# Kernel optimization log

Measured on AMD Instinct MI355X. Metric: run time of the kernel, lower is better.

The kernel has to match this reference:

```python
import jax, jax.numpy as jnp
import numpy as np

B, N, C, NH = 8, 16384, 256, 8
CH = C // NH          # head dim = 32
SCALE = CH ** -0.5
HH = WW = 128         # N = HH*WW
# CoaT crpe window dict {3:2, 5:3, 7:3}: 2 heads->3x3, 3 heads->5x5, 3 heads->7x7


def setup_inputs() -> dict:
    key = jax.random.key(0)
    ks = jax.random.split(key, 9)
    w = lambda k, shp: (jax.random.normal(k, shp, jnp.float32) * 0.02)
    return {
        "x": jax.random.normal(ks[0], (B, N, C), jnp.float32),
        "w_qkv": w(ks[1], (C, 3 * C)),              # qkv_bias=False
        "w_proj": w(ks[2], (C, C)),
        "b_proj": jnp.zeros((C,), jnp.float32),
        "w3": w(ks[3], (3, 3, 1, 2 * CH)),          # HWIO depthwise, 2 heads
        "b3": jnp.zeros((2 * CH,), jnp.float32),
        "w5": w(ks[4], (5, 5, 1, 3 * CH)),          # 3 heads
        "b5": jnp.zeros((3 * CH,), jnp.float32),
        "w7": w(ks[5], (7, 7, 1, 3 * CH)),          # 3 heads
        "b7": jnp.zeros((3 * CH,), jnp.float32),
        "H": HH,
        "W": WW,
    }


def _hydra(q, k, v):
    # q,k,v: [B, h, N, Ch]; normalize over feature dim, O(N) token reduction
    qn = q * jax.lax.rsqrt(jnp.sum(q * q, axis=-1, keepdims=True))
    kn = k * jax.lax.rsqrt(jnp.sum(k * k, axis=-1, keepdims=True))
    kv = jnp.sum(kn * v, axis=-2, keepdims=True)   # [B, h, 1, Ch]
    return qn * kv                                  # broadcast over tokens


def _dwconv(img, kern, bias):
    # img: [B, c, H, W]; kern: [kh, kw, 1, c] (HWIO depthwise)
    c = img.shape[1]
    out = jax.lax.conv_general_dilated(
        img, kern, window_strides=(1, 1), padding="SAME",
        feature_group_count=c,
        dimension_numbers=("NCHW", "HWIO", "NCHW"))
    return out + bias[None, :, None, None]


def _crpe(q, v, Hs, Ws, convs):
    # CoaT ConvRelPosEnc: depthwise conv on v per head group, gated by q
    b, h, n, ch = v.shape
    outs, idx = [], 0
    for heads, kern, bias in convs:
        vs = v[:, idx:idx + heads]                          # [B, hs, N, Ch]
        v_img = vs.transpose(0, 1, 3, 2).reshape(b, heads * ch, Hs, Ws)
        cv = _dwconv(v_img, kern, bias)
        cv = cv.reshape(b, heads, ch, n).transpose(0, 1, 3, 2)
        outs.append(q[:, idx:idx + heads] * cv)
        idx += heads
    return jnp.concatenate(outs, axis=1)                    # [B, h, N, Ch]


def reference(x, w_qkv, w_proj, b_proj, w3, b3, w5, b5, w7, b7, H, W):
    b, n, c = x.shape
    qkv = (x @ w_qkv).reshape(b, n, 3, NH, CH).transpose(2, 0, 3, 1, 4)
    q, k, v = qkv[0], qkv[1], qkv[2]                        # [B, h, N, Ch]
    factor_att = _hydra(q, k, v)
    crpe = _crpe(q, v, H, W, [(2, w3, b3), (3, w5, b5), (3, w7, b7)])
    out = SCALE * factor_att + crpe
    out = out.transpose(0, 2, 1, 3).reshape(b, n, c)        # [B, N, C]
    return out @ w_proj + b_proj
```

## Files before the change

kernel.cpp:

```cpp
#include <hip/hip_runtime.h>
#include <hip/hip_bf16.h>


typedef __hip_bfloat16 bf16;
typedef __bf16 bf16x8 __attribute__((ext_vector_type(8)));
typedef unsigned short u16x8 __attribute__((ext_vector_type(8)));
typedef float f32x4 __attribute__((ext_vector_type(4)));
typedef float f32x8 __attribute__((ext_vector_type(8)));

#define SCALE_ 0.17677669529663687f

__device__ __forceinline__ unsigned short f2b(float f) {
  __hip_bfloat16 h = __float2bfloat16(f);
  return __builtin_bit_cast(unsigned short, h);
}
__device__ __forceinline__ float blo(unsigned u) {
  return __builtin_bit_cast(float, u << 16);
}
__device__ __forceinline__ float bhi(unsigned u) {
  return __builtin_bit_cast(float, u & 0xffff0000u);
}
__device__ __forceinline__ f32x8 unpack8(uint4 u) {
  f32x8 r;
  r[0] = blo(u.x); r[1] = bhi(u.x); r[2] = blo(u.y); r[3] = bhi(u.y);
  r[4] = blo(u.z); r[5] = bhi(u.z); r[6] = blo(u.w); r[7] = bhi(u.w);
  return r;
}
__device__ __forceinline__ uint4 pack8(float a0, float a1, float a2, float a3,
                                       float a4, float a5, float a6, float a7) {
  uint4 s;
  s.x = (unsigned)f2b(a0) | ((unsigned)f2b(a1) << 16);
  s.y = (unsigned)f2b(a2) | ((unsigned)f2b(a3) << 16);
  s.z = (unsigned)f2b(a4) | ((unsigned)f2b(a5) << 16);
  s.w = (unsigned)f2b(a6) | ((unsigned)f2b(a7) << 16);
  return s;
}
__device__ __forceinline__ void gload16(const void* g, void* l) {
  __builtin_amdgcn_global_load_lds(
      (const __attribute__((address_space(1))) unsigned int*)g,
      (__attribute__((address_space(3))) unsigned int*)l, 16, 0, 0);
}
__device__ __forceinline__ f32x4 mfma16(u16x8 a, u16x8 b, f32x4 c) {
  return __builtin_amdgcn_mfma_f32_16x16x32_bf16(
      __builtin_bit_cast(bf16x8, a), __builtin_bit_cast(bf16x8, b), c, 0, 0, 0);
}

__global__ __launch_bounds__(256) void prep_weights(
    const float* __restrict__ wqkv, const float* __restrict__ wproj,
    bf16* __restrict__ wqkvT, bf16* __restrict__ wprojT) {
  const int idx = blockIdx.x * 256 + threadIdx.x;
  if (idx < 768 * 256) {
    const int j = idx >> 8, k = idx & 255;
    wqkvT[idx] = __float2bfloat16(wqkv[k * 768 + j]);
  }
  if (idx < 256 * 256) {
    const int j = idx >> 8, k = idx & 255;
    wprojT[idx] = __float2bfloat16(wproj[k * 256 + j]);
  }
}

__global__ __launch_bounds__(256) void qkv_mfma(
    const float* __restrict__ x, const bf16* __restrict__ wT,
    bf16* __restrict__ qO, bf16* __restrict__ kO, bf16* __restrict__ vO) {
  __shared__ __align__(16) char As[16384];
  __shared__ __align__(16) char Bs[16384];
  const int tid = threadIdx.x;
  const int l = tid & 63, w = tid >> 6;
  const int wr = w >> 1, wc = w & 1;

  const int lin = blockIdx.y * 6 + blockIdx.x;
  const int xcd = lin & 7, qq = lin >> 3;
  const int jt = qq % 6;
  const int ttile = xcd * 128 + qq / 6;
  const int j0 = jt << 7;
  const int t0 = ttile << 7;

  f32x4 acc[4][4];
#pragma unroll
  for (int m = 0; m < 4; ++m)
#pragma unroll
    for (int t = 0; t < 4; ++t) acc[m][t] = (f32x4){0.f, 0.f, 0.f, 0.f};

  const int arow0 = w * 16 + (l >> 2), arow1 = arow0 + 64;
  const int asl = l & 3;
  const bf16* asrc0 = wT + (size_t)(j0 + arow0) * 256 + ((asl ^ (arow0 & 3)) << 3);
  const bf16* asrc1 = wT + (size_t)(j0 + arow1) * 256 + ((asl ^ (arow1 & 3)) << 3);
  const int ad0 = w * 1024;
  const int ad1 = 4096 + w * 1024;

  const int brow = tid >> 1, bkh = tid & 1;
  const float* xp = x + (size_t)(t0 + brow) * 256 + bkh * 16;
  const int bw0 = brow * 64 + (((bkh << 1) ^ (brow & 3)) << 4);
  const int bw1 = brow * 64 + ((((bkh << 1) | 1) ^ (brow & 3)) << 4);

  const int fr = l & 15;
  const int fs = ((l >> 4) ^ (l & 3)) << 4;

  {
    const float4 xa0 = *(const float4*)(xp);
    const float4 xa1 = *(const float4*)(xp + 4);
    const float4 xa2 = *(const float4*)(xp + 8);
    const float4 xa3 = *(const float4*)(xp + 12);
    gload16(asrc0, As + ad0);
    gload16(asrc1, As + ad1);
    u16x8 p0, p1;
    p0[0] = f2b(xa0.x); p0[1] = f2b(xa0.y); p0[2] = f2b(xa0.z); p0[3] = f2b(xa0.w);
    p0[4] = f2b(xa1.x); p0[5] = f2b(xa1.y); p0[6] = f2b(xa1.z); p0[7] = f2b(xa1.w);
    p1[0] = f2b(xa2.x); p1[1] = f2b(xa2.y); p1[2] = f2b(xa2.z); p1[3] = f2b(xa2.w);
    p1[4] = f2b(xa3.x); p1[5] = f2b(xa3.y); p1[6] = f2b(xa3.z); p1[7] = f2b(xa3.w);
    *(u16x8*)(Bs + bw0) = p0;
    *(u16x8*)(Bs + bw1) = p1;
  }
  __syncthreads();

  int cur = 0;
  for (int t = 0; t < 8; ++t) {
    const int kn = (t + 1) << 5;
    const int nxt = (cur ^ 1) << 13;
    float4 xa0, xa1, xa2, xa3;
    if (t < 7) {
      xa0 = *(const float4*)(xp + kn);
      xa1 = *(const float4*)(xp + kn + 4);
      xa2 = *(const float4*)(xp + kn + 8);
      xa3 = *(const float4*)(xp + kn + 12);
      gload16(asrc0 + kn, As + nxt + ad0);
      gload16(asrc1 + kn, As + nxt + ad1);
    }
    const char* Ac = As + (cur << 13);
    const char* Bc = Bs + (cur << 13);
    u16x8 af[4], bfv[4];
#pragma unroll
    for (int m = 0; m < 4; ++m)
      af[m] = *(const u16x8*)(Ac + (wr * 64 + m * 16 + fr) * 64 + fs);
#pragma unroll
    for (int tt = 0; tt < 4; ++tt)
      bfv[tt] = *(const u16x8*)(Bc + (wc * 64 + tt * 16 + fr) * 64 + fs);
#pragma unroll
    for (int m = 0; m < 4; ++m)
#pragma unroll
      for (int tt = 0; tt < 4; ++tt)
        acc[m][tt] = mfma16(af[m], bfv[tt], acc[m][tt]);
    if (t < 7) {
      u16x8 p0, p1;
      p0[0] = f2b(xa0.x); p0[1] = f2b(xa0.y); p0[2] = f2b(xa0.z); p0[3] = f2b(xa0.w);
      p0[4] = f2b(xa1.x); p0[5] = f2b(xa1.y); p0[6] = f2b(xa1.z); p0[7] = f2b(xa1.w);
      p1[0] = f2b(xa2.x); p1[1] = f2b(xa2.y); p1[2] = f2b(xa2.z); p1[3] = f2b(xa2.w);
      p1[4] = f2b(xa3.x); p1[5] = f2b(xa3.y); p1[6] = f2b(xa3.z); p1[7] = f2b(xa3.w);
      *(u16x8*)(Bs + nxt + bw0) = p0;
      *(u16x8*)(Bs + nxt + bw1) = p1;
    }
    __syncthreads();
    cur ^= 1;
  }

  const int region = j0 >> 8;
  bf16* outp = (region == 0) ? qO : ((region == 1) ? kO : vO);
  const int b = t0 >> 14;
  const int n0 = (t0 & 16383) + wc * 64;
  const int fq = l >> 4;
  const int jl = (j0 & 255) + wr * 64;
#pragma unroll
  for (int m = 0; m < 4; ++m) {
    const int j = jl + m * 16 + fq * 4;
#pragma unroll
    for (int t = 0; t < 4; ++t) {
      const int n = n0 + t * 16 + fr;
      uint2 pk;
      pk.x = (unsigned)f2b(acc[m][t][0]) | ((unsigned)f2b(acc[m][t][1]) << 16);
      pk.y = (unsigned)f2b(acc[m][t][2]) | ((unsigned)f2b(acc[m][t][3]) << 16);
      *(uint2*)&outp[((size_t)b * 16384 + n) * 256 + j] = pk;
    }
  }
}

__global__ __launch_bounds__(256) void kv_reduce(
    const bf16* __restrict__ kT, const bf16* __restrict__ vT,
    float* __restrict__ kv) {
  const int tid = threadIdx.x;
  const int bh = blockIdx.y;
  const int b = bh >> 3, h = bh & 7;
  f32x8 part[4];
#pragma unroll
  for (int cc = 0; cc < 4; ++cc) part[cc] = (f32x8)0.f;

  for (int it = 0; it < 4; ++it) {
    const int n = blockIdx.x * 1024 + it * 256 + tid;
    const size_t off = ((size_t)b * 16384 + n) * 256 + h * 32;
    const uint4* kp = (const uint4*)(kT + off);
    const uint4* vp = (const uint4*)(vT + off);
    f32x8 kf[4];
    float ss = 0.f;
#pragma unroll
    for (int cc = 0; cc < 4; ++cc) {
      kf[cc] = unpack8(kp[cc]);
#pragma unroll
      for (int i = 0; i < 8; ++i) ss += kf[cc][i] * kf[cc][i];
    }
    const float inv = rsqrtf(ss);
#pragma unroll
    for (int cc = 0; cc < 4; ++cc) {
      f32x8 vf = unpack8(vp[cc]);
#pragma unroll
      for (int i = 0; i < 8; ++i) part[cc][i] += kf[cc][i] * inv * vf[i];
    }
  }
#pragma unroll
  for (int cc = 0; cc < 4; ++cc)
#pragma unroll
    for (int i = 0; i < 8; ++i) {
      float p = part[cc][i];
#pragma unroll
      for (int off = 32; off >= 1; off >>= 1) p += __shfl_xor(p, off);
      part[cc][i] = p;
    }
  if ((tid & 63) == 0) {
#pragma unroll
    for (int cc = 0; cc < 4; ++cc)
#pragma unroll
      for (int i = 0; i < 8; ++i)
        atomicAdd(&kv[bh * 32 + cc * 8 + i], part[cc][i]);
  }
}

template <int K>
__global__ __launch_bounds__(256) void crpe_conv(
    const bf16* __restrict__ qT, const bf16* __restrict__ vT,
    const float* __restrict__ kvbuf, const float* __restrict__ wp,
    const float* __restrict__ bp, int OC, int hbase,
    bf16* __restrict__ mid) {
  constexpr int R = K / 2;
  constexpr int S = 16 + 2 * R;
  constexpr int NSLOT = 4 * ((S - 1) * 23 + 1);
  __shared__ __align__(16) char vs[NSLOT * 16];
  __shared__ float wlds[K * K * 32];
  __shared__ float blds[32];

  const int tid = threadIdx.x;
  const int hg = blockIdx.x;
  const int h = hbase + hg;
  const int tile = blockIdx.y;
  const int b = blockIdx.z;
  const int tx0 = (tile & 7) * 16, ty0 = (tile >> 3) * 16;
  const int px = tid & 15, py = tid >> 4;
  const int ocbase = hg * 32;

  for (int e = tid; e < S * S; e += 256) {
    const int ly = e / S, lx = e - ly * S;
    const int gy = ty0 - R + ly, gx = tx0 - R + lx;
    uint4 d0 = {0, 0, 0, 0}, d1 = {0, 0, 0, 0}, d2 = {0, 0, 0, 0},
          d3 = {0, 0, 0, 0};
    if (gy >= 0 && gy < 128 && gx >= 0 && gx < 128) {
      const uint4* src = (const uint4*)(vT +
          ((size_t)b * 16384 + gy * 128 + gx) * 256 + h * 32);
      d0 = src[0]; d1 = src[1]; d2 = src[2]; d3 = src[3];
    }
    const int p = ly * 22 + lx;
    const int sw = (p >> 1) & 3;
    char* base = vs + ((p << 2) << 4);
    *(uint4*)(base + ((0 ^ sw) << 4)) = d0;
    *(uint4*)(base + ((1 ^ sw) << 4)) = d1;
    *(uint4*)(base + ((2 ^ sw) << 4)) = d2;
    *(uint4*)(base + ((3 ^ sw) << 4)) = d3;
  }
  for (int e = tid; e < K * K * 32; e += 256)
    wlds[e] = wp[(e >> 5) * OC + ocbase + (e & 31)];
  if (tid < 32) blds[tid] = bp[ocbase + tid];
  __syncthreads();

  const float4* bl4 = (const float4*)blds;
  f32x8 acc[4];
#pragma unroll
  for (int cc = 0; cc < 4; ++cc) {
    const float4 b0 = bl4[cc * 2], b1 = bl4[cc * 2 + 1];
    acc[cc][0] = b0.x; acc[cc][1] = b0.y; acc[cc][2] = b0.z; acc[cc][3] = b0.w;
    acc[cc][4] = b1.x; acc[cc][5] = b1.y; acc[cc][6] = b1.z; acc[cc][7] = b1.w;
  }
  const float4* wlds4 = (const float4*)wlds;
#pragma unroll 1
  for (int ky = 0; ky < K; ++ky) {
#pragma unroll
    for (int kx = 0; kx < K; ++kx) {
      const int p = (py + ky) * 22 + (px + kx);
      const int tap = ky * K + kx;
      const int sw = (p >> 1) & 3;
      const char* base = vs + ((p << 2) << 4);
#pragma unroll
      for (int cc = 0; cc < 4; ++cc) {
        const uint4 vv = *(const uint4*)(base + ((cc ^ sw) << 4));
        const f32x8 vf = unpack8(vv);
        const float4 w0 = wlds4[tap * 8 + cc * 2];
        const float4 w1 = wlds4[tap * 8 + cc * 2 + 1];
        acc[cc][0] += vf[0] * w0.x; acc[cc][1] += vf[1] * w0.y;
        acc[cc][2] += vf[2] * w0.z; acc[cc][3] += vf[3] * w0.w;
        acc[cc][4] += vf[4] * w1.x; acc[cc][5] += vf[5] * w1.y;
        acc[cc][6] += vf[6] * w1.z; acc[cc][7] += vf[7] * w1.w;
      }
    }
  }

  const int n = (ty0 + py) * 128 + (tx0 + px);
  const size_t off = ((size_t)b * 16384 + n) * 256 + h * 32;
  const uint4* qsrc = (const uint4*)(qT + off);
  f32x8 qv[4];
  float ss = 0.f;
#pragma unroll
  for (int cc = 0; cc < 4; ++cc) {
    qv[cc] = unpack8(qsrc[cc]);
#pragma unroll
    for (int i = 0; i < 8; ++i) ss += qv[cc][i] * qv[cc][i];
  }
  const float qinv = rsqrtf(ss);
  const float4* kvp = (const float4*)(kvbuf + ((size_t)b * 8 + h) * 32);
  uint4* mdst = (uint4*)(mid + off);
#pragma unroll
  for (int cc = 0; cc < 4; ++cc) {
    const float4 ka = kvp[cc * 2], kb = kvp[cc * 2 + 1];
    float o[8];
    o[0] = SCALE_ * qv[cc][0] * qinv * ka.x + qv[cc][0] * acc[cc][0];
    o[1] = SCALE_ * qv[cc][1] * qinv * ka.y + qv[cc][1] * acc[cc][1];
    o[2] = SCALE_ * qv[cc][2] * qinv * ka.z + qv[cc][2] * acc[cc][2];
    o[3] = SCALE_ * qv[cc][3] * qinv * ka.w + qv[cc][3] * acc[cc][3];
    o[4] = SCALE_ * qv[cc][4] * qinv * kb.x + qv[cc][4] * acc[cc][4];
    o[5] = SCALE_ * qv[cc][5] * qinv * kb.y + qv[cc][5] * acc[cc][5];
    o[6] = SCALE_ * qv[cc][6] * qinv * kb.z + qv[cc][6] * acc[cc][6];
    o[7] = SCALE_ * qv[cc][7] * qinv * kb.w + qv[cc][7] * acc[cc][7];
    mdst[cc] = pack8(o[0], o[1], o[2], o[3], o[4], o[5], o[6], o[7]);
  }
}

__global__ __launch_bounds__(256) void proj_mfma(
    const bf16* __restrict__ mid, const bf16* __restrict__ wpT,
    const float* __restrict__ bproj, float* __restrict__ out) {
  __shared__ __align__(16) char As[16384];
  __shared__ __align__(16) char Bs[16384];
  const int tid = threadIdx.x;
  const int l = tid & 63, w = tid >> 6;
  const int wr = w >> 1, wc = w & 1;

  const int lin = blockIdx.y * 2 + blockIdx.x;
  const int xcd = lin & 7, qq = lin >> 3;
  const int jt = qq & 1;
  const int ttile = xcd * 128 + (qq >> 1);
  const int j0 = jt << 7;
  const int tk0 = ttile << 7;

  f32x4 acc[4][4];
#pragma unroll
  for (int m = 0; m < 4; ++m)
#pragma unroll
    for (int t = 0; t < 4; ++t) acc[m][t] = (f32x4){0.f, 0.f, 0.f, 0.f};

  const int row0 = w * 16 + (l >> 2), row1 = row0 + 64;
  const int sl = l & 3;
  const bf16* asrc0 = wpT + (size_t)(j0 + row0) * 256 + ((sl ^ (row0 & 3)) << 3);
  const bf16* asrc1 = wpT + (size_t)(j0 + row1) * 256 + ((sl ^ (row1 & 3)) << 3);
  const bf16* bsrc0 = mid + (size_t)(tk0 + row0) * 256 + ((sl ^ (row0 & 3)) << 3);
  const bf16* bsrc1 = mid + (size_t)(tk0 + row1) * 256 + ((sl ^ (row1 & 3)) << 3);
  const int d0 = w * 1024;
  const int d1 = 4096 + w * 1024;

  const int fr = l & 15;
  const int fs = ((l >> 4) ^ (l & 3)) << 4;

  gload16(asrc0, As + d0);
  gload16(asrc1, As + d1);
  gload16(bsrc0, Bs + d0);
  gload16(bsrc1, Bs + d1);
  __syncthreads();

  int cur = 0;
  for (int t = 0; t < 8; ++t) {
    const int kn = (t + 1) << 5;
    const int nxt = (cur ^ 1) << 13;
    if (t < 7) {
      gload16(asrc0 + kn, As + nxt + d0);
      gload16(asrc1 + kn, As + nxt + d1);
      gload16(bsrc0 + kn, Bs + nxt + d0);
      gload16(bsrc1 + kn, Bs + nxt + d1);
    }
    const char* Ac = As + (cur << 13);
    const char* Bc = Bs + (cur << 13);
    u16x8 af[4], bfv[4];
#pragma unroll
    for (int m = 0; m < 4; ++m)
      af[m] = *(const u16x8*)(Ac + (wr * 64 + m * 16 + fr) * 64 + fs);
#pragma unroll
    for (int tt = 0; tt < 4; ++tt)
      bfv[tt] = *(const u16x8*)(Bc + (wc * 64 + tt * 16 + fr) * 64 + fs);
#pragma unroll
    for (int m = 0; m < 4; ++m)
#pragma unroll
      for (int tt = 0; tt < 4; ++tt)
        acc[m][tt] = mfma16(af[m], bfv[tt], acc[m][tt]);
    __syncthreads();
    cur ^= 1;
  }

  const int fq = l >> 4;
#pragma unroll
  for (int m = 0; m < 4; ++m) {
    const int j = j0 + wr * 64 + m * 16 + fq * 4;
    const float4 bias = *(const float4*)&bproj[j];
#pragma unroll
    for (int t = 0; t < 4; ++t) {
      const int token = tk0 + wc * 64 + t * 16 + fr;
      float4 r;
      r.x = acc[m][t][0] + bias.x;
      r.y = acc[m][t][1] + bias.y;
      r.z = acc[m][t][2] + bias.z;
      r.w = acc[m][t][3] + bias.w;
      *(float4*)&out[(size_t)token * 256 + j] = r;
    }
  }
}

extern "C" void kernel_launch(void* const* d_in, const int* in_sizes, int n_in,
                              void* d_out, int out_size, void* d_ws,
                              size_t ws_size, hipStream_t stream) {
  const float* x     = (const float*)d_in[0];
  const float* wqkv  = (const float*)d_in[1];
  const float* wproj = (const float*)d_in[2];
  const float* bproj = (const float*)d_in[3];
  const float* w3 = (const float*)d_in[4];
  const float* b3 = (const float*)d_in[5];
  const float* w5 = (const float*)d_in[6];
  const float* b5 = (const float*)d_in[7];
  const float* w7 = (const float*)d_in[8];
  const float* b7 = (const float*)d_in[9];
  float* out = (float*)d_out;

  const size_t PLANE = (size_t)8 * 16384 * 256;
  bf16* qT  = (bf16*)d_ws;
  bf16* vT  = qT + PLANE;
  bf16* kT  = vT + PLANE;
  bf16* mid = kT;
  float* kv = (float*)(kT + PLANE);
  bf16* wqkvT  = (bf16*)(kv + 2048);
  bf16* wprojT = wqkvT + 768 * 256;

  hipMemsetAsync(kv, 0, 2048 * sizeof(float), stream);
  prep_weights<<<dim3(768), 256, 0, stream>>>(wqkv, wproj, wqkvT, wprojT);
  qkv_mfma<<<dim3(6, 1024), 256, 0, stream>>>(x, wqkvT, qT, kT, vT);
  kv_reduce<<<dim3(16, 64), 256, 0, stream>>>(kT, vT, kv);
  crpe_conv<3><<<dim3(2, 64, 8), 256, 0, stream>>>(qT, vT, kv, w3, b3, 64, 0, mid);
  crpe_conv<5><<<dim3(3, 64, 8), 256, 0, stream>>>(qT, vT, kv, w5, b5, 96, 2, mid);
  crpe_conv<7><<<dim3(3, 64, 8), 256, 0, stream>>>(qT, vT, kv, w7, b7, 96, 5, mid);
  proj_mfma<<<dim3(2, 1024), 256, 0, stream>>>(mid, wprojT, bproj, out);
}
```

Baseline: 420.6 us.

## Stage GEMM epilogues through LDS for coalesced stores; coalesce kv_reduce loads

The QKV and projection GEMM epilogues now write accumulators into a swizzled LDS tile and read them back so each thread emits full 16-byte contiguous row stores, replacing scattered 8/16-byte column fragments. The LDS swizzle for operand tiles is changed to use (row>>1)&3 to reduce bank conflicts. kv_reduce is restructured so each warp reads whole 512-byte token rows across all heads, with per-head norms via shuffles and an LDS tree reduction before the atomics. This adds an extra LDS round trip and barriers in the epilogues.

```diff
diff --git a/kernel.cpp b/kernel.cpp
--- a/kernel.cpp
+++ b/kernel.cpp
@@ -62,8 +62,9 @@
 __global__ __launch_bounds__(256) void qkv_mfma(
     const float* __restrict__ x, const bf16* __restrict__ wT,
     bf16* __restrict__ qO, bf16* __restrict__ kO, bf16* __restrict__ vO) {
-  __shared__ __align__(16) char As[16384];
-  __shared__ __align__(16) char Bs[16384];
+  __shared__ __align__(16) char LDSU[32768];
+  char* As = LDSU;
+  char* Bs = LDSU + 16384;
   const int tid = threadIdx.x;
   const int l = tid & 63, w = tid >> 6;
   const int wr = w >> 1, wc = w & 1;
@@ -83,18 +84,22 @@
 
   const int arow0 = w * 16 + (l >> 2), arow1 = arow0 + 64;
   const int asl = l & 3;
-  const bf16* asrc0 = wT + (size_t)(j0 + arow0) * 256 + ((asl ^ (arow0 & 3)) << 3);
-  const bf16* asrc1 = wT + (size_t)(j0 + arow1) * 256 + ((asl ^ (arow1 & 3)) << 3);
+  const bf16* asrc0 =
+      wT + (size_t)(j0 + arow0) * 256 + ((asl ^ ((arow0 >> 1) & 3)) << 3);
+  const bf16* asrc1 =
+      wT + (size_t)(j0 + arow1) * 256 + ((asl ^ ((arow1 >> 1) & 3)) << 3);
   const int ad0 = w * 1024;
   const int ad1 = 4096 + w * 1024;
 
   const int brow = tid >> 1, bkh = tid & 1;
   const float* xp = x + (size_t)(t0 + brow) * 256 + bkh * 16;
-  const int bw0 = brow * 64 + (((bkh << 1) ^ (brow & 3)) << 4);
-  const int bw1 = brow * 64 + ((((bkh << 1) | 1) ^ (brow & 3)) << 4);
+  const int bsw = (brow >> 1) & 3;
+  const int bw0 = brow * 64 + (((bkh << 1) ^ bsw) << 4);
+  const int bw1 = brow * 64 + ((((bkh << 1) | 1) ^ bsw) << 4);
 
   const int fr = l & 15;
-  const int fs = ((l >> 4) ^ (l & 3)) << 4;
+  const int fq = l >> 4;
+  const int fs = (fq ^ ((l >> 1) & 3)) << 4;
 
   {
     const float4 xa0 = *(const float4*)(xp);
@@ -153,72 +158,78 @@
     cur ^= 1;
   }
 
+#pragma unroll
+  for (int m = 0; m < 4; ++m) {
+    const int jq = wr * 16 + m * 4 + fq;
+#pragma unroll
+    for (int t = 0; t < 4; ++t) {
+      const int token = wc * 64 + t * 16 + fr;
+      const int p = jq ^ (token & 15);
+      uint2 pk;
+      pk.x = (unsigned)f2b(acc[m][t][0]) | ((unsigned)f2b(acc[m][t][1]) << 16);
+      pk.y = (unsigned)f2b(acc[m][t][2]) | ((unsigned)f2b(acc[m][t][3]) << 16);
+      *(uint2*)(LDSU + token * 256 + (p << 3)) = pk;
+    }
+  }
+  __syncthreads();
+
   const int region = j0 >> 8;
   bf16* outp = (region == 0) ? qO : ((region == 1) ? kO : vO);
   const int b = t0 >> 14;
-  const int n0 = (t0 & 16383) + wc * 64;
-  const int fq = l >> 4;
-  const int jl = (j0 & 255) + wr * 64;
-#pragma unroll
-  for (int m = 0; m < 4; ++m) {
-    const int j = jl + m * 16 + fq * 4;
-#pragma unroll
-    for (int t = 0; t < 4; ++t) {
-      const int n = n0 + t * 16 + fr;
-      uint2 pk;
-      pk.x = (unsigned)f2b(acc[m][t][0]) | ((unsigned)f2b(acc[m][t][1]) << 16);
-      pk.y = (unsigned)f2b(acc[m][t][2]) | ((unsigned)f2b(acc[m][t][3]) << 16);
-      *(uint2*)&outp[((size_t)b * 16384 + n) * 256 + j] = pk;
-    }
+  const int n0 = t0 & 16383;
+  const int jl = j0 & 255;
+  const int seg = tid & 15;
+#pragma unroll
+  for (int r = 0; r < 8; ++r) {
+    const int token = r * 16 + (tid >> 4);
+    const int tsw = token & 15;
+    const int q0 = (2 * seg) ^ tsw;
+    const int q1 = (2 * seg + 1) ^ tsw;
+    const uint2 lo = *(const uint2*)(LDSU + token * 256 + (q0 << 3));
+    const uint2 hi = *(const uint2*)(LDSU + token * 256 + (q1 << 3));
+    uint4 d;
+    d.x = lo.x; d.y = lo.y; d.z = hi.x; d.w = hi.y;
+    *(uint4*)&outp[((size_t)b * 16384 + n0 + token) * 256 + jl + seg * 8] = d;
   }
 }
 
 __global__ __launch_bounds__(256) void kv_reduce(
     const bf16* __restrict__ kT, const bf16* __restrict__ vT,
     float* __restrict__ kv) {
+  __shared__ float red[256 * 8];
   const int tid = threadIdx.x;
-  const int bh = blockIdx.y;
-  const int b = bh >> 3, h = bh & 7;
-  f32x8 part[4];
-#pragma unroll
-  for (int cc = 0; cc < 4; ++cc) part[cc] = (f32x8)0.f;
-
-  for (int it = 0; it < 4; ++it) {
-    const int n = blockIdx.x * 1024 + it * 256 + tid;
-    const size_t off = ((size_t)b * 16384 + n) * 256 + h * 32;
-    const uint4* kp = (const uint4*)(kT + off);
-    const uint4* vp = (const uint4*)(vT + off);
-    f32x8 kf[4];
+  const int b = blockIdx.y;
+  const int seg = tid & 31;
+  f32x8 part = (f32x8)0.f;
+
+  for (int r = 0; r < 32; ++r) {
+    const int token = blockIdx.x * 256 + r * 8 + (tid >> 5);
+    const size_t roff = ((size_t)b * 16384 + token) * 256;
+    const uint4 kd = *(const uint4*)(kT + roff + seg * 8);
+    const f32x8 kf = unpack8(kd);
     float ss = 0.f;
 #pragma unroll
-    for (int cc = 0; cc < 4; ++cc) {
-      kf[cc] = unpack8(kp[cc]);
-#pragma unroll
-      for (int i = 0; i < 8; ++i) ss += kf[cc][i] * kf[cc][i];
-    }
+    for (int i = 0; i < 8; ++i) ss += kf[i] * kf[i];
+    ss += __shfl_xor(ss, 1);
+    ss += __shfl_xor(ss, 2);
     const float inv = rsqrtf(ss);
-#pragma unroll
-    for (int cc = 0; cc < 4; ++cc) {
-      f32x8 vf = unpack8(vp[cc]);
-#pragma unroll
-      for (int i = 0; i < 8; ++i) part[cc][i] += kf[cc][i] * inv * vf[i];
-    }
-  }
-#pragma unroll
-  for (int cc = 0; cc < 4; ++cc)
-#pragma unroll
-    for (int i = 0; i < 8; ++i) {
-      float p = part[cc][i];
-#pragma unroll
-      for (int off = 32; off >= 1; off >>= 1) p += __shfl_xor(p, off);
-      part[cc][i] = p;
-    }
-  if ((tid & 63) == 0) {
-#pragma unroll
-    for (int cc = 0; cc < 4; ++cc)
-#pragma unroll
-      for (int i = 0; i < 8; ++i)
-        atomicAdd(&kv[bh * 32 + cc * 8 + i], part[cc][i]);
+    const uint4 vd = *(const uint4*)(vT + roff + seg * 8);
+    const f32x8 vf = unpack8(vd);
+#pragma unroll
+    for (int i = 0; i < 8; ++i) part[i] += kf[i] * inv * vf[i];
+  }
+#pragma unroll
+  for (int i = 0; i < 8; ++i) red[tid * 8 + i] = part[i];
+  __syncthreads();
+  if (tid < 32) {
+    f32x8 s = (f32x8)0.f;
+#pragma unroll
+    for (int k = 0; k < 8; ++k)
+#pragma unroll
+      for (int i = 0; i < 8; ++i) s[i] += red[(tid + 32 * k) * 8 + i];
+#pragma unroll
+    for (int i = 0; i < 8; ++i)
+      atomicAdd(&kv[b * 256 + seg * 8 + i], s[i]);
   }
 }
 
@@ -331,8 +342,9 @@
 __global__ __launch_bounds__(256) void proj_mfma(
     const bf16* __restrict__ mid, const bf16* __restrict__ wpT,
     const float* __restrict__ bproj, float* __restrict__ out) {
-  __shared__ __align__(16) char As[16384];
-  __shared__ __align__(16) char Bs[16384];
+  __shared__ __align__(16) char LDSU[32768];
+  char* As = LDSU;
+  char* Bs = LDSU + 16384;
   const int tid = threadIdx.x;
   const int l = tid & 63, w = tid >> 6;
   const int wr = w >> 1, wc = w & 1;
@@ -352,15 +364,17 @@
 
   const int row0 = w * 16 + (l >> 2), row1 = row0 + 64;
   const int sl = l & 3;
-  const bf16* asrc0 = wpT + (size_t)(j0 + row0) * 256 + ((sl ^ (row0 & 3)) << 3);
-  const bf16* asrc1 = wpT + (size_t)(j0 + row1) * 256 + ((sl ^ (row1 & 3)) << 3);
-  const bf16* bsrc0 = mid + (size_t)(tk0 + row0) * 256 + ((sl ^ (row0 & 3)) << 3);
-  const bf16* bsrc1 = mid + (size_t)(tk0 + row1) * 256 + ((sl ^ (row1 & 3)) << 3);
+  const int sw0 = (row0 >> 1) & 3, sw1 = (row1 >> 1) & 3;
+  const bf16* asrc0 = wpT + (size_t)(j0 + row0) * 256 + ((sl ^ sw0) << 3);
+  const bf16* asrc1 = wpT + (size_t)(j0 + row1) * 256 + ((sl ^ sw1) << 3);
+  const bf16* bsrc0 = mid + (size_t)(tk0 + row0) * 256 + ((sl ^ sw0) << 3);
+  const bf16* bsrc1 = mid + (size_t)(tk0 + row1) * 256 + ((sl ^ sw1) << 3);
   const int d0 = w * 1024;
   const int d1 = 4096 + w * 1024;
 
   const int fr = l & 15;
-  const int fs = ((l >> 4) ^ (l & 3)) << 4;
+  const int fq = l >> 4;
+  const int fs = (fq ^ ((l >> 1) & 3)) << 4;
 
   gload16(asrc0, As + d0);
   gload16(asrc1, As + d1);
@@ -396,21 +410,44 @@
     cur ^= 1;
   }
 
-  const int fq = l >> 4;
 #pragma unroll
   for (int m = 0; m < 4; ++m) {
-    const int j = j0 + wr * 64 + m * 16 + fq * 4;
-    const float4 bias = *(const float4*)&bproj[j];
+    const float4 bias = *(const float4*)&bproj[j0 + wr * 64 + m * 16 + fq * 4];
 #pragma unroll
     for (int t = 0; t < 4; ++t) {
-      const int token = tk0 + wc * 64 + t * 16 + fr;
-      float4 r;
-      r.x = acc[m][t][0] + bias.x;
-      r.y = acc[m][t][1] + bias.y;
-      r.z = acc[m][t][2] + bias.z;
-      r.w = acc[m][t][3] + bias.w;
-      *(float4*)&out[(size_t)token * 256 + j] = r;
-    }
+      acc[m][t][0] += bias.x;
+      acc[m][t][1] += bias.y;
+      acc[m][t][2] += bias.z;
+      acc[m][t][3] += bias.w;
+    }
+  }
+
+  for (int chunk = 0; chunk < 2; ++chunk) {
+    if (wc == chunk) {
+#pragma unroll
+      for (int m = 0; m < 4; ++m) {
+        const int jq = wr * 16 + m * 4 + fq;
+#pragma unroll
+        for (int t = 0; t < 4; ++t) {
+          const int ltok = t * 16 + fr;
+          const int p = jq ^ (ltok & 15);
+          float4 r;
+          r.x = acc[m][t][0]; r.y = acc[m][t][1];
+          r.z = acc[m][t][2]; r.w = acc[m][t][3];
+          *(float4*)(LDSU + ltok * 512 + (p << 4)) = r;
+        }
+      }
+    }
+    __syncthreads();
+    const int seg = tid & 31;
+#pragma unroll
+    for (int r = 0; r < 8; ++r) {
+      const int ltok = r * 8 + (tid >> 5);
+      const int p = seg ^ (ltok & 15);
+      const float4 dv = *(const float4*)(LDSU + ltok * 512 + (p << 4));
+      *(float4*)&out[(size_t)(tk0 + chunk * 64 + ltok) * 256 + j0 + seg * 4] = dv;
+    }
+    __syncthreads();
   }
 }
 
@@ -441,7 +478,7 @@
   hipMemsetAsync(kv, 0, 2048 * sizeof(float), stream);
   prep_weights<<<dim3(768), 256, 0, stream>>>(wqkv, wproj, wqkvT, wprojT);
   qkv_mfma<<<dim3(6, 1024), 256, 0, stream>>>(x, wqkvT, qT, kT, vT);
-  kv_reduce<<<dim3(16, 64), 256, 0, stream>>>(kT, vT, kv);
+  kv_reduce<<<dim3(64, 8), 256, 0, stream>>>(kT, vT, kv);
   crpe_conv<3><<<dim3(2, 64, 8), 256, 0, stream>>>(qT, vT, kv, w3, b3, 64, 0, mid);
   crpe_conv<5><<<dim3(3, 64, 8), 256, 0, stream>>>(qT, vT, kv, w5, b5, 96, 2, mid);
   crpe_conv<7><<<dim3(3, 64, 8), 256, 0, stream>>>(qT, vT, kv, w7, b7, 96, 5, mid);
```

Result: faster. 344.8 us (-18.0%).
